# Kernel optimization log

Hardware: AMD Instinct MI355X
Metric: run time of the kernel (lower is better)

## Reference

```python
import jax, jax.numpy as jnp
import numpy as np

HEAD_DIM = 128
N_HEADS = 16
N_KV_HEADS = 4
N_REP = N_HEADS // N_KV_HEADS


def _rope(x, cos, sin):
    # x: [B, S, Hk, D]; cos/sin: [S, D/2]
    xr = x.reshape(*x.shape[:-1], -1, 2)
    x0, x1 = xr[..., 0], xr[..., 1]
    c = cos[None, :, None, :]
    s = sin[None, :, None, :]
    o0 = x0 * c - x1 * s
    o1 = x0 * s + x1 * c
    return jnp.stack([o0, o1], axis=-1).reshape(x.shape)


def setup_inputs() -> dict:
    key = jax.random.key(0)
    ks = jax.random.split(key, 7)
    B, S, DIM = 2, 1024, 2048
    KV_DIM = HEAD_DIM * N_KV_HEADS
    x = jax.random.normal(ks[0], (B, S, DIM), dtype=jnp.float32)
    # rotary angles like LLaMA: freqs = 1/10000^(2i/D)
    inv_freq = 1.0 / (10000.0 ** (np.arange(0, HEAD_DIM, 2, dtype=np.float32) / HEAD_DIM))
    ang = np.arange(S, dtype=np.float32)[:, None] * inv_freq[None, :]  # [S, D/2]
    theta_cos = jnp.asarray(np.cos(ang))
    theta_sin = jnp.asarray(np.sin(ang))
    sc = 0.02
    wq = jax.random.normal(ks[1], (DIM, DIM), dtype=jnp.float32) * sc
    wk = jax.random.normal(ks[2], (DIM, KV_DIM), dtype=jnp.float32) * sc
    wv = jax.random.normal(ks[3], (DIM, KV_DIM), dtype=jnp.float32) * sc
    wo = jax.random.normal(ks[4], (DIM, DIM), dtype=jnp.float32) * sc
    return {"x": x, "theta_cos": theta_cos, "theta_sin": theta_sin,
            "wq": wq, "wk": wk, "wv": wv, "wo": wo}


def reference(x, theta_cos, theta_sin, wq, wk, wv, wo):
    B, S, DIM = x.shape
    # projections
    xq = (x @ wq).reshape(B, S, N_HEADS, HEAD_DIM).transpose(0, 2, 1, 3)  # [B,H,S,D]
    xk = (x @ wk).reshape(B, S, N_KV_HEADS, HEAD_DIM)                      # [B,S,Hk,D]
    xv = (x @ wv).reshape(B, S, N_KV_HEADS, HEAD_DIM)
    # RoPE on K and V only (faithful to source: Q is NOT rotated)
    xk = _rope(xk, theta_cos, theta_sin)
    xv = _rope(xv, theta_cos, theta_sin)
    # GQA repeat: [B,S,Hk,D] -> [B,H,S,D] (each kv head repeated consecutively)
    xk = jnp.repeat(xk.transpose(0, 2, 1, 3), N_REP, axis=1)
    xv = jnp.repeat(xv.transpose(0, 2, 1, 3), N_REP, axis=1)
    scale = HEAD_DIM ** (-0.5)
    att = jnp.einsum('bhqd,bhkd->bhqk', xq, xk) * scale
    # faithful masking: tril then masked_fill(att == 0, -inf)
    tri = jnp.tril(jnp.ones((S, S), dtype=bool))
    att = jnp.where(tri[None, None], att, 0.0)
    att = jnp.where(att == 0.0, -jnp.inf, att)
    att = jax.nn.softmax(att, axis=-1)
    y = jnp.einsum('bhqk,bhkd->bhqd', att, xv)
    out = y.transpose(0, 2, 1, 3).reshape(B, S, DIM)
    return out @ wo
```

## Files before the change

kernel.cpp:

```cpp
#include <hip/hip_runtime.h>
#include <hip/hip_bf16.h>
#include <stdint.h>
#include <math.h>

typedef _Float16 half_t;
typedef __attribute__((ext_vector_type(2))) _Float16 h2_t;
typedef __attribute__((ext_vector_type(4))) _Float16 h4_t;
typedef __attribute__((ext_vector_type(8))) _Float16 h8_t;
typedef __attribute__((ext_vector_type(4))) float f32x4;
typedef __attribute__((ext_vector_type(4))) uint32_t u32x4;

#if __has_builtin(__builtin_amdgcn_exp2f)
#define EXP2(x) __builtin_amdgcn_exp2f(x)
#else
#define EXP2(x) exp2f(x)
#endif

__device__ __forceinline__ void gload16(const void* g, void* l) {
    __builtin_amdgcn_global_load_lds(
        (const __attribute__((address_space(1))) uint32_t*)(uintptr_t)g,
        (__attribute__((address_space(3))) uint32_t*)(uint32_t)(uintptr_t)l,
        16, 0, 0);
}

__global__ __launch_bounds__(256) void prep(const float* __restrict__ x, half_t* __restrict__ xh,
                                            const float* __restrict__ wq, const float* __restrict__ wk,
                                            const float* __restrict__ wv, const float* __restrict__ wo,
                                            half_t* __restrict__ qt, half_t* __restrict__ kt,
                                            half_t* __restrict__ vt, half_t* __restrict__ ot) {
    __shared__ half_t T[32][36];
    const int bx = blockIdx.x;
    if (bx < 2048) {
        int g = (bx * 256 + threadIdx.x) * 8;
        float4 a = *(const float4*)(x + g);
        float4 b = *(const float4*)(x + g + 4);
        h8_t o = {(half_t)a.x,(half_t)a.y,(half_t)a.z,(half_t)a.w,
                  (half_t)b.x,(half_t)b.y,(half_t)b.z,(half_t)b.w};
        *(h8_t*)(xh + g) = o;
        return;
    }
    const int wb = bx - 2048;
    const float* src; half_t* dst; int Nd, t;
    if (wb < 4096)      { src = wq; dst = qt; Nd = 2048; t = wb; }
    else if (wb < 5120) { src = wk; dst = kt; Nd = 512;  t = wb - 4096; }
    else if (wb < 6144) { src = wv; dst = vt; Nd = 512;  t = wb - 5120; }
    else                { src = wo; dst = ot; Nd = 2048; t = wb - 6144; }
    const int K = 2048;
    int nt = Nd >> 5;
    int ti = t / nt, tj = t % nt;
    int r  = threadIdx.x >> 3;
    int c4 = (threadIdx.x & 7) << 2;
    float4 v = *(const float4*)(src + (size_t)(ti*32 + r) * Nd + tj*32 + c4);
    T[r][c4+0] = (half_t)v.x; T[r][c4+1] = (half_t)v.y;
    T[r][c4+2] = (half_t)v.z; T[r][c4+3] = (half_t)v.w;
    __syncthreads();
    h4_t o = {T[c4+0][r], T[c4+1][r], T[c4+2][r], T[c4+3][r]};
    *(h4_t*)(dst + (size_t)(tj*32 + r) * K + ti*32 + c4) = o;
}

template<int QKV, typename CT>
__global__ __launch_bounds__(256) void gemm_t(const half_t* __restrict__ A,
                                              const half_t* __restrict__ Bq,
                                              const half_t* __restrict__ Bk,
                                              const half_t* __restrict__ Bv,
                                              CT* __restrict__ Cq,
                                              half_t* __restrict__ Ck,
                                              half_t* __restrict__ Vt,
                                              const float* __restrict__ Cs,
                                              const float* __restrict__ Sn,
                                              int NB, int K) {
    constexpr int BM  = 64;
    constexpr int MI  = 2;
    constexpr int ACH = 8;
    constexpr int PW  = 6;
    __shared__ half_t SMEM[2 * (64 + 128) * 64];
    half_t* A0 = SMEM;
    half_t* B0 = SMEM + 64 * 64;
    half_t* A1 = SMEM + 192 * 64;
    half_t* B1 = A1 + 64 * 64;
    const int tid = threadIdx.x, lane = tid & 63, wid = tid >> 6;
    const int lr = lane & 15, lg = lane >> 4;
    const int wm = wid >> 1, wn = wid & 1;
    const int bid = blockIdx.x;
    const int xcd   = bid & 7;
    const int local = bid >> 3;
    const int perx  = NB >> 3;
    const int bn = perx * xcd + local % perx;
    const int bm = local / perx;
    const int m0 = bm * BM;

    const half_t* W; CT* Cc; int cs, col0;
    if constexpr (QKV) {
        if (bn < 16)      { W = Bq + (size_t)bn * 128 * K;        Cc = Cq;       cs = 2048; col0 = bn * 128; }
        else if (bn < 20) { W = Bk + (size_t)(bn - 16) * 128 * K; Cc = (CT*)Ck;  cs = 512;  col0 = (bn - 16) * 128; }
        else              { W = Bv + (size_t)(bn - 20) * 128 * K; Cc = (CT*)Ck;  cs = 512;  col0 = (bn - 20) * 128; }
    } else {
        W = Bq + (size_t)bn * 128 * K; Cc = Cq; cs = NB * 128; col0 = bn * 128;
    }

    const half_t* Arow = A + (size_t)m0 * K;
    f32x4 acc[MI][4] = {};

    auto stage = [&](half_t* Ah, half_t* Bh, int k0) {
        #pragma unroll
        for (int c = 0; c < PW; c++) {
            const int chunk = wid * PW + c;
            const int o = lane * 16;
            if (chunk < ACH) {
                const int go   = (chunk << 10) + o;
                const int row  = go >> 7;
                const int colb = (go & 127) ^ ((row & 7) << 4);
                gload16(Arow + (size_t)row * K + k0 + (colb >> 1), (char*)Ah + (chunk << 10));
            } else {
                const int go   = ((chunk - ACH) << 10) + o;
                const int row  = go >> 7;
                const int colb = (go & 127) ^ ((row & 7) << 4);
                gload16(W + (size_t)row * K + k0 + (colb >> 1), (char*)Bh + ((chunk - ACH) << 10));
            }
        }
    };

    auto compute = [&](const half_t* Ah, const half_t* Bh) {
        h8_t af[2][MI], bf[2][4];
        #pragma unroll
        for (int kk = 0; kk < 2; kk++) {
            #pragma unroll
            for (int mi = 0; mi < MI; mi++) {
                const int row = wm * 32 + mi * 16 + lr;
                const int cb  = (kk * 64 + lg * 16) ^ ((lr & 7) << 4);
                af[kk][mi] = *(const h8_t*)((const char*)Ah + row * 128 + cb);
            }
            #pragma unroll
            for (int ni = 0; ni < 4; ni++) {
                const int row = wn * 64 + ni * 16 + lr;
                const int cb  = (kk * 64 + lg * 16) ^ ((lr & 7) << 4);
                bf[kk][ni] = *(const h8_t*)((const char*)Bh + row * 128 + cb);
            }
        }
        #pragma unroll
        for (int kk = 0; kk < 2; kk++)
            #pragma unroll
            for (int mi = 0; mi < MI; mi++)
                #pragma unroll
                for (int ni = 0; ni < 4; ni++)
                    acc[mi][ni] = __builtin_amdgcn_mfma_f32_16x16x32_f16(af[kk][mi], bf[kk][ni], acc[mi][ni], 0, 0, 0);
    };

    stage(A0, B0, 0);
    __syncthreads();
    for (int k0 = 0; k0 < K; k0 += 128) {
        stage(A1, B1, k0 + 64);
        compute(A0, B0);
        __syncthreads();
        if (k0 + 128 < K) stage(A0, B0, k0 + 128);
        compute(A1, B1);
        __syncthreads();
    }

    if constexpr (QKV) {
        if (bn >= 16) {
            #pragma unroll
            for (int ni = 0; ni < 4; ni++) {
                const int dh  = wn * 64 + ni * 16 + lr;
                const int p   = dh >> 1;
                const float sg = (lr & 1) ? 1.f : -1.f;
                #pragma unroll
                for (int mi = 0; mi < MI; mi++)
                    #pragma unroll
                    for (int r = 0; r < 4; r++) {
                        const int row = m0 + wm * 32 + mi * 16 + lg * 4 + r;
                        const int s = row & 1023;
                        const float c  = Cs[s * 64 + p];
                        const float si = Sn[s * 64 + p];
                        const float own = acc[mi][ni][r];
                        const float par = __shfl_xor(own, 1);
                        acc[mi][ni][r] = own * c + par * (sg * si);
                    }
            }
            if (bn >= 20) {
                __syncthreads();
                half_t* T = SMEM;
                constexpr int LD = 68;
                #pragma unroll
                for (int mi = 0; mi < MI; mi++)
                    #pragma unroll
                    for (int ni = 0; ni < 4; ni++) {
                        const int d  = wn * 64 + ni * 16 + lr;
                        const int s0 = wm * 32 + mi * 16 + lg * 4;
                        h4_t o = {(half_t)acc[mi][ni][0], (half_t)acc[mi][ni][1],
                                  (half_t)acc[mi][ni][2], (half_t)acc[mi][ni][3]};
                        *(h4_t*)(T + d * LD + s0) = o;
                    }
                __syncthreads();
                #pragma unroll
                for (int it = 0; it < 4; it++) {
                    const int d  = it * 32 + (tid >> 3);
                    const int c8 = (tid & 7) * 8;
                    h8_t o;
                    #pragma unroll
                    for (int e = 0; e < 8; e++) o[e] = T[d * LD + c8 + e];
                    *(h8_t*)(Vt + (size_t)(col0 + d) * 2048 + m0 + c8) = o;
                }
                return;
            }
        }
    }

    #pragma unroll
    for (int mi = 0; mi < MI; mi++)
        #pragma unroll
        for (int ni = 0; ni < 4; ni++)
            #pragma unroll
            for (int r = 0; r < 4; r++) {
                int row = m0 + wm * 32 + mi * 16 + lg * 4 + r;
                int col = col0 + wn * 64 + ni * 16 + lr;
                Cc[(size_t)row * cs + col] = (CT)acc[mi][ni][r];
            }
}

__global__ __launch_bounds__(256, 3) void attn9(const half_t* __restrict__ Qh,
                                                const half_t* __restrict__ Kh,
                                                const half_t* __restrict__ Vtg,
                                                half_t* __restrict__ Yh,
                                                half_t* __restrict__ Yp,
                                                float* __restrict__ ML) {
    __shared__ half_t K0[64 * 128];
    __shared__ half_t V0[128 * 64];

    const int tid = threadIdx.x, lane = tid & 63, wid = tid >> 6;
    const int lr = lane & 15, lg = lane >> 4;
    const int bx = blockIdx.x;
    const int g  = bx & 7;
    const int local = bx >> 3;
    const int b = g >> 2, kvh = g & 3;
    const int h = kvh * 4 + (local & 3);
    const int pp = local >> 2;
    int qt, kb0, kb1, part; bool partial;
    if (pp < 8)       { qt = 8 + pp;      kb0 = 0; kb1 = 7;  partial = true;  part = 0; }
    else if (pp < 16) { qt = pp - 8;      kb0 = 0; kb1 = qt; partial = false; part = 0; }
    else              { qt = 15-(pp-16);  kb0 = 8; kb1 = qt; partial = true;  part = 1; }

    const int qbase = qt * 64 + wid * 16;
    const int q     = qbase + lr;
    const size_t kbase = (size_t)b * 1024;

    const float sc2 = 0.08838834764831845f * 1.4426950408889634f;
    h8_t qf[4];
    #pragma unroll
    for (int kk = 0; kk < 4; kk++) {
        qf[kk] = *(const h8_t*)(Qh + ((size_t)(b * 1024) + q) * 2048 + h * 128 + kk * 32 + lg * 8);
        qf[kk] = qf[kk] * (half_t)sc2;
    }

    float m = -1e30f, l = 0.f;
    f32x4 yacc[8] = {};

    {
        const int j = kb0 * 64;
        #pragma unroll
        for (int c = 0; c < 4; c++) {
            const int chunk = wid * 4 + c;
            const int o = (chunk << 10) + lane * 16;
            { const int row  = o >> 8;
              const int colb = (o & 255) ^ ((row & 7) << 4);
              gload16(Kh + (kbase + j + row) * 512 + kvh * 128 + (colb >> 1),
                      (char*)K0 + (chunk << 10)); }
            { const int row  = o >> 7;
              const int colb = (o & 127) ^ ((row & 7) << 4);
              gload16(Vtg + (size_t)(kvh * 128 + row) * 2048 + kbase + j + (colb >> 1),
                      (char*)V0 + (chunk << 10)); }
        }
    }
    __syncthreads();

    for (int kb = kb0; kb <= kb1; kb++) {
        const bool pf = (kb + 1 <= kb1);
        h8_t kpre[4], vpre[4];
        if (pf) {
            const int j2 = (kb + 1) * 64;
            #pragma unroll
            for (int c = 0; c < 4; c++) {
                const int chunk = wid * 4 + c;
                const int o = (chunk << 10) + lane * 16;
                { const int row  = o >> 8;
                  const int colb = (o & 255) ^ ((row & 7) << 4);
                  kpre[c] = *(const h8_t*)(Kh + (kbase + j2 + row) * 512 + kvh * 128 + (colb >> 1)); }
                { const int row  = o >> 7;
                  const int colb = (o & 127) ^ ((row & 7) << 4);
                  vpre[c] = *(const h8_t*)(Vtg + (size_t)(kvh * 128 + row) * 2048 + kbase + j2 + (colb >> 1)); }
            }
        }

        const int j = kb * 64;
        f32x4 st[4] = {};
        __builtin_amdgcn_s_setprio(1);
        #pragma unroll
        for (int t4 = 0; t4 < 4; t4++)
            #pragma unroll
            for (int kk = 0; kk < 4; kk++) {
                const int row = t4 * 16 + lr;
                const int cb  = (kk * 64 + lg * 16) ^ ((lr & 7) << 4);
                h8_t kf = *(const h8_t*)((const char*)K0 + row * 256 + cb);
                st[t4] = __builtin_amdgcn_mfma_f32_16x16x32_f16(kf, qf[kk], st[t4], 0, 0, 0);
            }
        __builtin_amdgcn_s_setprio(0);
        if (kb == qt) {
            #pragma unroll
            for (int t4 = 0; t4 < 4; t4++)
                #pragma unroll
                for (int r = 0; r < 4; r++)
                    if (j + t4 * 16 + lg * 4 + r > q) st[t4][r] = -1e30f;
        }
        float mb = fmaxf(fmaxf(fmaxf(st[0][0], st[0][1]), fmaxf(st[0][2], st[0][3])),
                         fmaxf(fmaxf(st[1][0], st[1][1]), fmaxf(st[1][2], st[1][3])));
        mb = fmaxf(mb, fmaxf(fmaxf(fmaxf(st[2][0], st[2][1]), fmaxf(st[2][2], st[2][3])),
                             fmaxf(fmaxf(st[3][0], st[3][1]), fmaxf(st[3][2], st[3][3]))));
        mb = fmaxf(mb, __shfl_xor(mb, 16));
        mb = fmaxf(mb, __shfl_xor(mb, 32));
        if (!__all(mb - m <= 8.0f)) {
            float mn = fmaxf(m, mb);
            float al = EXP2(m - mn);
            m = mn;
            l *= al;
            #pragma unroll
            for (int dt = 0; dt < 8; dt++)
                #pragma unroll
                for (int r = 0; r < 4; r++)
                    yacc[dt][r] *= al;
        }
        float rs = 0.f;
        #pragma unroll
        for (int t4 = 0; t4 < 4; t4++)
            #pragma unroll
            for (int r = 0; r < 4; r++) {
                float p = EXP2(st[t4][r] - m);
                st[t4][r] = p;
                rs += p;
            }
        rs += __shfl_xor(rs, 16);
        rs += __shfl_xor(rs, 32);
        l += rs;
        uint32_t h2p[4][2];
        #pragma unroll
        for (int t4 = 0; t4 < 4; t4++) {
            h2p[t4][0] = __builtin_bit_cast(uint32_t,
                __builtin_amdgcn_cvt_pkrtz(st[t4][0], st[t4][1]));
            h2p[t4][1] = __builtin_bit_cast(uint32_t,
                __builtin_amdgcn_cvt_pkrtz(st[t4][2], st[t4][3]));
        }
        const int src1 = ((lg & 1) << 5) + lr;
        const int src2 = src1 + 16;
        const bool sel = (lg < 2);
        h8_t pb[2];
        #pragma unroll
        for (int c = 0; c < 2; c++) {
            uint32_t lo0 = __shfl((int)h2p[2*c][0],   src1);
            uint32_t lo1 = __shfl((int)h2p[2*c][1],   src1);
            uint32_t lo2 = __shfl((int)h2p[2*c][0],   src2);
            uint32_t lo3 = __shfl((int)h2p[2*c][1],   src2);
            uint32_t hi0 = __shfl((int)h2p[2*c+1][0], src1);
            uint32_t hi1 = __shfl((int)h2p[2*c+1][1], src1);
            uint32_t hi2 = __shfl((int)h2p[2*c+1][0], src2);
            uint32_t hi3 = __shfl((int)h2p[2*c+1][1], src2);
            u32x4 w = { sel ? lo0 : hi0, sel ? lo1 : hi1,
                        sel ? lo2 : hi2, sel ? lo3 : hi3 };
            pb[c] = __builtin_bit_cast(h8_t, w);
        }
        __builtin_amdgcn_s_setprio(1);
        #pragma unroll
        for (int dt = 0; dt < 8; dt++) {
            const int row = dt * 16 + lr;
            const int cb0 = (lg * 16) ^ ((lr & 7) << 4);
            const int cb1 = (64 + lg * 16) ^ ((lr & 7) << 4);
            h8_t v0 = *(const h8_t*)((const char*)V0 + row * 128 + cb0);
            h8_t v1 = *(const h8_t*)((const char*)V0 + row * 128 + cb1);
            yacc[dt] = __builtin_amdgcn_mfma_f32_16x16x32_f16(v0, pb[0], yacc[dt], 0, 0, 0);
            yacc[dt] = __builtin_amdgcn_mfma_f32_16x16x32_f16(v1, pb[1], yacc[dt], 0, 0, 0);
        }
        __builtin_amdgcn_s_setprio(0);

        __syncthreads();
        if (pf) {
            #pragma unroll
            for (int c = 0; c < 4; c++) {
                const int chunk = wid * 4 + c;
                const int o = (chunk << 10) + lane * 16;
                *(h8_t*)((char*)K0 + o) = kpre[c];
                *(h8_t*)((char*)V0 + o) = vpre[c];
            }
            __syncthreads();
        }
    }

    const float inv = 1.0f / l;
    if (!partial) {
        #pragma unroll
        for (int dt = 0; dt < 8; dt++) {
            h4_t o = {(half_t)(yacc[dt][0] * inv), (half_t)(yacc[dt][1] * inv),
                      (half_t)(yacc[dt][2] * inv), (half_t)(yacc[dt][3] * inv)};
            *(h4_t*)(Yh + ((size_t)(b * 1024) + q) * 2048 + h * 128 + dt * 16 + lg * 4) = o;
        }
    } else {
        const int pidx = ((b * 16 + h) * 8 + (qt - 8)) * 2 + part;
        half_t* yp = Yp + (size_t)pidx * 8192;
        const int rl = wid * 16 + lr;
        #pragma unroll
        for (int dt = 0; dt < 8; dt++) {
            h4_t o = {(half_t)(yacc[dt][0] * inv), (half_t)(yacc[dt][1] * inv),
                      (half_t)(yacc[dt][2] * inv), (half_t)(yacc[dt][3] * inv)};
            *(h4_t*)(yp + rl * 128 + dt * 16 + lg * 4) = o;
        }
        if (lg == 0) {
            float* ml = ML + (size_t)pidx * 128;
            ml[rl]      = m;
            ml[64 + rl] = l;
        }
    }
}

__global__ __launch_bounds__(256) void merge2(const half_t* __restrict__ Yp,
                                              const float* __restrict__ ML,
                                              half_t* __restrict__ Yh) {
    const int sidx = blockIdx.x;
    const int b = sidx >> 7;
    const int rem = sidx & 127;
    const int h = rem >> 3;
    const int qt = 8 + (rem & 7);
    const int t = threadIdx.x;
    const int row = t >> 2;
    const int cg = (t & 3) * 32;
    const float* ml0 = ML + (size_t)(sidx * 2) * 128;
    const float* ml1 = ml0 + 128;
    const float m0 = ml0[row], l0 = ml0[64 + row];
    const float m1 = ml1[row], l1 = ml1[64 + row];
    const float M  = fmaxf(m0, m1);
    const float w0 = l0 * EXP2(m0 - M), w1 = l1 * EXP2(m1 - M);
    const float inv = 1.0f / (w0 + w1);
    const float a0 = w0 * inv, a1 = w1 * inv;
    const half_t* y0 = Yp + (size_t)(sidx * 2) * 8192 + row * 128 + cg;
    const half_t* y1 = y0 + 8192;
    half_t* out = Yh + ((size_t)(b * 1024 + qt * 64 + row)) * 2048 + h * 128 + cg;
    #pragma unroll
    for (int c = 0; c < 32; c += 8) {
        h8_t u = *(const h8_t*)(y0 + c);
        h8_t v = *(const h8_t*)(y1 + c);
        h8_t o;
        #pragma unroll
        for (int e = 0; e < 8; e++)
            o[e] = (half_t)(a0 * (float)u[e] + a1 * (float)v[e]);
        *(h8_t*)(out + c) = o;
    }
}

extern "C" void kernel_launch(void* const* d_in, const int* in_sizes, int n_in,
                              void* d_out, int out_size, void* d_ws, size_t ws_size,
                              hipStream_t stream) {
    const float* x  = (const float*)d_in[0];
    const float* tc = (const float*)d_in[1];
    const float* ts = (const float*)d_in[2];
    const float* wq = (const float*)d_in[3];
    const float* wk = (const float*)d_in[4];
    const float* wv = (const float*)d_in[5];
    const float* wo = (const float*)d_in[6];
    float* out = (float*)d_out;

    const size_t MD = 2048ull * 2048, MK = 2048ull * 512;
    half_t* Xh  = (half_t*)d_ws;
    half_t* Qh  = Xh  + MD;
    half_t* Kh  = Qh  + MD;
    half_t* Vh  = Kh  + MK;
    half_t* Vt  = Vh  + MK;
    half_t* Yh  = Vt  + MK;
    half_t* wqt = Yh  + MD;
    half_t* wkt = wqt + MD;
    half_t* wvt = wkt + MK;
    half_t* wot = wvt + MK;
    half_t* Yp  = wot + MD;
    float*  ML  = (float*)(Yp + 512ull * 8192);

    prep<<<12288, 256, 0, stream>>>(x, Xh, wq, wk, wv, wo, wqt, wkt, wvt, wot);
    gemm_t<1, half_t><<<768, 256, 0, stream>>>(Xh, wqt, wkt, wvt, Qh, Kh, Vt, tc, ts, 24, 2048);
    attn9<<<768, 256, 0, stream>>>(Qh, Kh, Vt, Yh, Yp, ML);
    merge2<<<256, 256, 0, stream>>>(Yp, ML, Yh);
    gemm_t<0, float><<<512, 256, 0, stream>>>(Yh, wot, nullptr, nullptr, out, nullptr, nullptr, nullptr, nullptr, 16, 2048);
}
```

Measured before the change: 102.1 us.

## Double-buffer K/V tiles in LDS with async global-to-LDS loads in attention

Replaces the register-staged prefetch of K/V tiles (global load into registers, then write to LDS after a barrier) with two LDS buffers filled directly by global_load_lds while the other buffer is being computed on. This removes the register round-trip and one barrier per iteration and frees VGPRs used for the prefetch. LDS per block doubles to 64KB and launch bounds drop from 3 to 2 blocks per CU, which may reduce occupancy. The correctness of the async loads relies on the single barrier after each iteration covering both load completion and buffer reuse.

New measurement: 104.8 us. 1.03x slower.

```diff
diff --git a/kernel.cpp b/kernel.cpp
--- a/kernel.cpp
+++ b/kernel.cpp
@@ -218,14 +218,14 @@
             }
 }
 
-__global__ __launch_bounds__(256, 3) void attn9(const half_t* __restrict__ Qh,
-                                                const half_t* __restrict__ Kh,
-                                                const half_t* __restrict__ Vtg,
-                                                half_t* __restrict__ Yh,
-                                                half_t* __restrict__ Yp,
-                                                float* __restrict__ ML) {
-    __shared__ half_t K0[64 * 128];
-    __shared__ half_t V0[128 * 64];
+__global__ __launch_bounds__(256, 2) void attn10(const half_t* __restrict__ Qh,
+                                                 const half_t* __restrict__ Kh,
+                                                 const half_t* __restrict__ Vtg,
+                                                 half_t* __restrict__ Yh,
+                                                 half_t* __restrict__ Yp,
+                                                 float* __restrict__ ML) {
+    __shared__ half_t K0[64 * 128], V0[128 * 64];
+    __shared__ half_t K1[64 * 128], V1[128 * 64];
 
     const int tid = threadIdx.x, lane = tid & 63, wid = tid >> 6;
     const int lr = lane & 15, lg = lane >> 4;
@@ -255,8 +255,8 @@
     float m = -1e30f, l = 0.f;
     f32x4 yacc[8] = {};
 
-    {
-        const int j = kb0 * 64;
+    auto stage = [&](half_t* kt, half_t* vb, int kb) {
+        const int j = kb * 64;
         #pragma unroll
         for (int c = 0; c < 4; c++) {
             const int chunk = wid * 4 + c;
@@ -264,33 +264,15 @@
             { const int row  = o >> 8;
               const int colb = (o & 255) ^ ((row & 7) << 4);
               gload16(Kh + (kbase + j + row) * 512 + kvh * 128 + (colb >> 1),
-                      (char*)K0 + (chunk << 10)); }
+                      (char*)kt + (chunk << 10)); }
             { const int row  = o >> 7;
               const int colb = (o & 127) ^ ((row & 7) << 4);
               gload16(Vtg + (size_t)(kvh * 128 + row) * 2048 + kbase + j + (colb >> 1),
-                      (char*)V0 + (chunk << 10)); }
-        }
-    }
-    __syncthreads();
-
-    for (int kb = kb0; kb <= kb1; kb++) {
-        const bool pf = (kb + 1 <= kb1);
-        h8_t kpre[4], vpre[4];
-        if (pf) {
-            const int j2 = (kb + 1) * 64;
-            #pragma unroll
-            for (int c = 0; c < 4; c++) {
-                const int chunk = wid * 4 + c;
-                const int o = (chunk << 10) + lane * 16;
-                { const int row  = o >> 8;
-                  const int colb = (o & 255) ^ ((row & 7) << 4);
-                  kpre[c] = *(const h8_t*)(Kh + (kbase + j2 + row) * 512 + kvh * 128 + (colb >> 1)); }
-                { const int row  = o >> 7;
-                  const int colb = (o & 127) ^ ((row & 7) << 4);
-                  vpre[c] = *(const h8_t*)(Vtg + (size_t)(kvh * 128 + row) * 2048 + kbase + j2 + (colb >> 1)); }
-            }
-        }
-
+                      (char*)vb + (chunk << 10)); }
+        }
+    };
+
+    auto iter = [&](const half_t* kt, const half_t* vb, int kb) {
         const int j = kb * 64;
         f32x4 st[4] = {};
         __builtin_amdgcn_s_setprio(1);
@@ -300,7 +282,7 @@
             for (int kk = 0; kk < 4; kk++) {
                 const int row = t4 * 16 + lr;
                 const int cb  = (kk * 64 + lg * 16) ^ ((lr & 7) << 4);
-                h8_t kf = *(const h8_t*)((const char*)K0 + row * 256 + cb);
+                h8_t kf = *(const h8_t*)((const char*)kt + row * 256 + cb);
                 st[t4] = __builtin_amdgcn_mfma_f32_16x16x32_f16(kf, qf[kk], st[t4], 0, 0, 0);
             }
         __builtin_amdgcn_s_setprio(0);
@@ -372,22 +354,23 @@
             const int row = dt * 16 + lr;
             const int cb0 = (lg * 16) ^ ((lr & 7) << 4);
             const int cb1 = (64 + lg * 16) ^ ((lr & 7) << 4);
-            h8_t v0 = *(const h8_t*)((const char*)V0 + row * 128 + cb0);
-            h8_t v1 = *(const h8_t*)((const char*)V0 + row * 128 + cb1);
+            h8_t v0 = *(const h8_t*)((const char*)vb + row * 128 + cb0);
+            h8_t v1 = *(const h8_t*)((const char*)vb + row * 128 + cb1);
             yacc[dt] = __builtin_amdgcn_mfma_f32_16x16x32_f16(v0, pb[0], yacc[dt], 0, 0, 0);
             yacc[dt] = __builtin_amdgcn_mfma_f32_16x16x32_f16(v1, pb[1], yacc[dt], 0, 0, 0);
         }
         __builtin_amdgcn_s_setprio(0);
-
+    };
+
+    stage(K0, V0, kb0);
+    __syncthreads();
+    for (int kb = kb0; kb <= kb1; kb += 2) {
+        if (kb + 1 <= kb1) stage(K1, V1, kb + 1);
+        iter(K0, V0, kb);
         __syncthreads();
-        if (pf) {
-            #pragma unroll
-            for (int c = 0; c < 4; c++) {
-                const int chunk = wid * 4 + c;
-                const int o = (chunk << 10) + lane * 16;
-                *(h8_t*)((char*)K0 + o) = kpre[c];
-                *(h8_t*)((char*)V0 + o) = vpre[c];
-            }
+        if (kb + 1 <= kb1) {
+            if (kb + 2 <= kb1) stage(K0, V0, kb + 2);
+            iter(K1, V1, kb + 1);
             __syncthreads();
         }
     }
@@ -480,7 +463,7 @@
 
     prep<<<12288, 256, 0, stream>>>(x, Xh, wq, wk, wv, wo, wqt, wkt, wvt, wot);
     gemm_t<1, half_t><<<768, 256, 0, stream>>>(Xh, wqt, wkt, wvt, Qh, Kh, Vt, tc, ts, 24, 2048);
-    attn9<<<768, 256, 0, stream>>>(Qh, Kh, Vt, Yh, Yp, ML);
+    attn10<<<768, 256, 0, stream>>>(Qh, Kh, Vt, Yh, Yp, ML);
     merge2<<<256, 256, 0, stream>>>(Yp, ML, Yh);
     gemm_t<0, float><<<512, 256, 0, stream>>>(Yh, wot, nullptr, nullptr, out, nullptr, nullptr, nullptr, nullptr, 16, 2048);
 }
```
